# Performance work log

Measured on AMD Instinct MI355X. Metric: run time of the kernel, lower is better.

## Reference

```python
import jax, jax.numpy as jnp
import numpy as np

B, H, S, D = 2, 8, 2048, 64

def setup_inputs() -> dict:
    key = jax.random.key(0)
    ks = jax.random.split(key, 6)
    names = ["Qx", "Kx", "Vx", "Qy", "Ky", "Vy"]
    return {n: jax.random.normal(k, (B, H, S, D), dtype=jnp.float32)
            for n, k in zip(names, ks)}

def reference(Qx, Kx, Vx, Qy, Ky, Vy):
    scale = float(np.sqrt(Qx.shape[-1]))
    # Two score matmuls: [B,H,S,S] each
    ax = jnp.einsum('bhqd,bhkd->bhqk', Qx, Kx)
    ay = jnp.einsum('bhqd,bhkd->bhqk', Qy, Ky)
    # cat(dim=1) -> reshape(B,2,H,S,S) -> mean(dim=1) == elementwise average
    attn = (ax + ay) * 0.5
    # numerically stable softmax over keys; dropout is identity in eval mode
    w = jax.nn.softmax(attn / scale, axis=-1)
    # Shared attention weights into two value matmuls
    out1 = jnp.einsum('bhqk,bhkd->bhqd', w, Vx)
    out2 = jnp.einsum('bhqk,bhkd->bhqd', w, Vy)
    return (out1, out2)
```

## Files before the change

kernel.cpp:

```cpp
#include <hip/hip_runtime.h>
#include <hip/hip_bf16.h>

typedef __attribute__((ext_vector_type(4)))  float f32x4;
typedef __attribute__((ext_vector_type(16))) float f32x16;
typedef __attribute__((ext_vector_type(8)))  short s16x8;
typedef __attribute__((ext_vector_type(4)))  short s16x4;
typedef __attribute__((ext_vector_type(4)))  int   i32x4;

#define BB 2
#define HH 8
#define SS 2048
#define DD 64
#define QBLK 128
#define NT   32
#define NT2  16
#define NBH  (BB * HH)

#define WS_KX 0
#define WS_KY ((size_t)NBH * NT * 8192)
#define WS_VX ((size_t)2 * NBH * NT * 8192)
#define WS_VY ((size_t)3 * NBH * NT * 8192)
#define WS_NEED ((size_t)4 * NBH * NT * 8192)

__device__ __forceinline__ short f2bf(float x) {
    unsigned u = __builtin_bit_cast(unsigned, x);
    u = (u + 0x7FFFu + ((u >> 16) & 1u)) >> 16;
    return (short)u;
}

__device__ __forceinline__ unsigned cvtpk(float lo, float hi) {
    unsigned d;
    asm("v_cvt_pk_bf16_f32 %0, %1, %2" : "=v"(d) : "v"(lo), "v"(hi));
    return d;
}

__device__ __forceinline__ int swz(int row, int byteInRow) {
    return row * 128 + (byteInRow ^ ((row & 7) << 4));
}

__device__ __forceinline__ void glds16(const void* g, void* l) {
    __builtin_amdgcn_global_load_lds(
        (const __attribute__((address_space(1))) unsigned*)g,
        (__attribute__((address_space(3))) unsigned*)l, 16, 0, 0);
}

__global__ __launch_bounds__(256)
void prep_kv(const float* __restrict__ Kx, const float* __restrict__ Ky,
             const float* __restrict__ Vx, const float* __restrict__ Vy,
             char* __restrict__ ws)
{
    const int b = blockIdx.x;
    if (b < 1024) {
        const int tid  = b * 256 + threadIdx.x;
        const int dblk = tid & 7;
        const int s    = (tid >> 3) & 2047;
        const int bh   = tid >> 14;
        const size_t gi = ((size_t)bh * SS + s) * DD + dblk * 8;
        const int kt = s >> 6, row = s & 63;
        const size_t dst = (size_t)(bh * NT + kt) * 8192 + swz(row, dblk * 16);
        const float* px = Kx + gi;
        const float* py = Ky + gi;
        s16x8 a, bb;
#pragma unroll
        for (int i = 0; i < 8; ++i) { a[i] = f2bf(px[i]); bb[i] = f2bf(py[i]); }
        *(s16x8*)(ws + WS_KX + dst) = a;
        *(s16x8*)(ws + WS_KY + dst) = bb;
    } else {
        const int tid  = (b - 1024) * 256 + threadIdx.x;
        const int d    = tid & 63;
        const int sblk = (tid >> 6) & 7;
        const int kt   = (tid >> 9) & 31;
        const int bh   = tid >> 14;
        const size_t gbase = ((size_t)bh * SS + kt * 64 + sblk * 8) * DD + d;
        s16x8 a, bb;
#pragma unroll
        for (int i = 0; i < 8; ++i) {
            a[i]  = f2bf(Vx[gbase + (size_t)i * DD]);
            bb[i] = f2bf(Vy[gbase + (size_t)i * DD]);
        }
        const size_t dst = (size_t)(bh * NT + kt) * 8192 + swz(d, sblk * 16);
        *(s16x8*)(ws + WS_VX + dst) = a;
        *(s16x8*)(ws + WS_VY + dst) = bb;
    }
}

__global__ __launch_bounds__(512, 2)
void attn_main(const float* __restrict__ Qx, const float* __restrict__ Qy,
               const char* __restrict__ ws, float* __restrict__ Out)
{
    extern __shared__ char lds[];

    const int t    = threadIdx.x;
    const int lane = t & 63;
    const int w    = t >> 6;
    const int qsub = w & 3;
    const int ks   = w >> 2;
    const int l31  = lane & 31;
    const int hi   = lane >> 5;

    int bid = blockIdx.x;
    bid = (bid & 7) * 32 + (bid >> 3);
    const int bh = bid >> 4;
    const int q0 = (bid & 15) * QBLK;
    const size_t base = (size_t)bh * SS * DD;

    const int qrow = q0 + qsub * 32 + l31;
    s16x8 qbx[4], qby[4];
#pragma unroll
    for (int dc = 0; dc < 4; ++dc) {
        const int d0 = dc * 16 + hi * 8;
        const float* qp = Qx + base + (size_t)qrow * DD + d0;
        const float* qq = Qy + base + (size_t)qrow * DD + d0;
        const float4 f0 = *(const float4*)qp;
        const float4 f1 = *(const float4*)(qp + 4);
        const float4 h0 = *(const float4*)qq;
        const float4 h1 = *(const float4*)(qq + 4);
        qbx[dc][0]=f2bf(f0.x); qbx[dc][1]=f2bf(f0.y); qbx[dc][2]=f2bf(f0.z); qbx[dc][3]=f2bf(f0.w);
        qbx[dc][4]=f2bf(f1.x); qbx[dc][5]=f2bf(f1.y); qbx[dc][6]=f2bf(f1.z); qbx[dc][7]=f2bf(f1.w);
        qby[dc][0]=f2bf(h0.x); qby[dc][1]=f2bf(h0.y); qby[dc][2]=f2bf(h0.z); qby[dc][3]=f2bf(h0.w);
        qby[dc][4]=f2bf(h1.x); qby[dc][5]=f2bf(h1.y); qby[dc][6]=f2bf(h1.z); qby[dc][7]=f2bf(h1.w);
    }

    f32x16 o1_0, o1_1, o2_0, o2_1;
#pragma unroll
    for (int j = 0; j < 16; ++j) { o1_0[j] = 0.f; o1_1[j] = 0.f; o2_0[j] = 0.f; o2_1[j] = 0.f; }
    float lsum = 0.f;

    const float SCL = 0.09016844005556021f;

#define STAGE(kt_, b_)                                                             \
    do {                                                                           \
        const size_t img_ = (size_t)(bh * NT + (kt_) * 2) * 8192 + (size_t)t * 16; \
        char* dst_ = lds + (b_) * 65536 + t * 16;                                  \
        glds16(ws + WS_KX + img_,        dst_);                                    \
        glds16(ws + WS_KX + img_ + 8192, dst_ + 8192);                             \
        glds16(ws + WS_KY + img_,        dst_ + 16384);                            \
        glds16(ws + WS_KY + img_ + 8192, dst_ + 24576);                            \
        glds16(ws + WS_VX + img_,        dst_ + 32768);                            \
        glds16(ws + WS_VX + img_ + 8192, dst_ + 40960);                            \
        glds16(ws + WS_VY + img_,        dst_ + 49152);                            \
        glds16(ws + WS_VY + img_ + 8192, dst_ + 57344);                            \
    } while (0)

#define QK_BLOCK(buf_, h_, sc_)                                                    \
    do {                                                                           \
        const char* KxI_ = (buf_) + ks * 8192;                                     \
        const char* KyI_ = (buf_) + 16384 + ks * 8192;                             \
        _Pragma("unroll")                                                          \
        for (int dc = 0; dc < 4; ++dc) {                                           \
            const int off = swz((h_) * 32 + l31, dc * 32 + hi * 16);               \
            const s16x8 ka = *(const s16x8*)(KxI_ + off);                          \
            const s16x8 kb = *(const s16x8*)(KyI_ + off);                          \
            sc_ = __builtin_amdgcn_mfma_f32_32x32x16_bf16(ka, qbx[dc], sc_, 0, 0, 0); \
            sc_ = __builtin_amdgcn_mfma_f32_32x32x16_bf16(kb, qby[dc], sc_, 0, 0, 0); \
        }                                                                          \
    } while (0)

#define V_READS(buf_, h_, vr_)                                                     \
    do {                                                                           \
        const char* VxI_ = (buf_) + 32768 + ks * 8192;                             \
        const char* VyI_ = (buf_) + 49152 + ks * 8192;                             \
        _Pragma("unroll")                                                          \
        for (int ch = 0; ch < 2; ++ch) {                                           \
            const int off0 = swz(l31,      (h_) * 64 + ch * 32 + hi * 16);         \
            const int off1 = swz(32 + l31, (h_) * 64 + ch * 32 + hi * 16);         \
            vr_[ch * 4 + 0] = *(const s16x8*)(VxI_ + off0);                        \
            vr_[ch * 4 + 1] = *(const s16x8*)(VxI_ + off1);                        \
            vr_[ch * 4 + 2] = *(const s16x8*)(VyI_ + off0);                        \
            vr_[ch * 4 + 3] = *(const s16x8*)(VyI_ + off1);                        \
        }                                                                          \
    } while (0)

#define SOFTMAX_PA(sc_, pa_)                                                       \
    do {                                                                           \
        float s_ = 0.f;                                                            \
        _Pragma("unroll")                                                          \
        for (int j = 0; j < 16; ++j) { sc_[j] = exp2f(sc_[j] * SCL); s_ += sc_[j]; } \
        lsum += s_;                                                                \
        _Pragma("unroll")                                                          \
        for (int ch = 0; ch < 2; ++ch) {                                           \
            const int b8 = ch * 8;                                                 \
            unsigned x0 = cvtpk(sc_[b8 + 0], sc_[b8 + 1]);                         \
            unsigned x1 = cvtpk(sc_[b8 + 2], sc_[b8 + 3]);                         \
            unsigned y0 = cvtpk(sc_[b8 + 4], sc_[b8 + 5]);                         \
            unsigned y1 = cvtpk(sc_[b8 + 6], sc_[b8 + 7]);                         \
            asm("v_permlane32_swap_b32 %0, %1" : "+v"(x0), "+v"(y0));              \
            asm("v_permlane32_swap_b32 %0, %1" : "+v"(x1), "+v"(y1));              \
            i32x4 pw;                                                              \
            pw[0] = (int)x0; pw[1] = (int)x1; pw[2] = (int)y0; pw[3] = (int)y1;    \
            pa_[ch] = __builtin_bit_cast(s16x8, pw);                               \
        }                                                                          \
    } while (0)

#define PV_BLOCK(pa_, vr_)                                                         \
    do {                                                                           \
        _Pragma("unroll")                                                          \
        for (int ch = 0; ch < 2; ++ch) {                                           \
            o1_0 = __builtin_amdgcn_mfma_f32_32x32x16_bf16(pa_[ch], vr_[ch*4+0], o1_0, 0, 0, 0); \
            o1_1 = __builtin_amdgcn_mfma_f32_32x32x16_bf16(pa_[ch], vr_[ch*4+1], o1_1, 0, 0, 0); \
            o2_0 = __builtin_amdgcn_mfma_f32_32x32x16_bf16(pa_[ch], vr_[ch*4+2], o2_0, 0, 0, 0); \
            o2_1 = __builtin_amdgcn_mfma_f32_32x32x16_bf16(pa_[ch], vr_[ch*4+3], o2_1, 0, 0, 0); \
        }                                                                          \
    } while (0)

#define ZERO16(v_) { _Pragma("unroll") for (int j = 0; j < 16; ++j) (v_)[j] = 0.f; }

    STAGE(0, 0);
    __syncthreads();
    int cur = 0;

    for (int kt = 0; kt < NT2; ++kt) {
        if (kt + 1 < NT2) STAGE(kt + 1, cur ^ 1);

        const char* buf = lds + cur * 65536;
        f32x16 scA, scB;
        ZERO16(scA); ZERO16(scB);
        s16x8 pa[2], vrA[8], vrB[8];

        __builtin_amdgcn_s_setprio(1);
        QK_BLOCK(buf, 0, scA);
        QK_BLOCK(buf, 1, scB);
        V_READS(buf, 0, vrA);
        SOFTMAX_PA(scA, pa);
        PV_BLOCK(pa, vrA);
        V_READS(buf, 1, vrB);
        SOFTMAX_PA(scB, pa);
        PV_BLOCK(pa, vrB);
        __builtin_amdgcn_s_setprio(0);

        __syncthreads();
        cur ^= 1;
    }

#undef STAGE
#undef QK_BLOCK
#undef V_READS
#undef SOFTMAX_PA
#undef PV_BLOCK
#undef ZERO16

    const float lh = lsum + __shfl_xor(lsum, 32);

    __syncthreads();
    float* ex   = (float*)lds;
    float* linv = (float*)(lds + 65536);
    const int exo = (qsub * 64 + lane) * 33;
    float* O1 = Out;
    float* O2 = Out + (size_t)BB * HH * SS * DD;

    if (ks == 1) {
#pragma unroll
        for (int j = 0; j < 16; ++j) { ex[exo + j] = o1_0[j]; ex[exo + 16 + j] = o1_1[j]; }
        ex[exo + 32] = lh;
    }
    __syncthreads();
    if (ks == 0 && hi == 0)
        linv[qsub * 32 + l31] = 1.0f / (lh + ex[exo + 32]);
    __syncthreads();
    if (ks == 0) {
#pragma unroll
        for (int j = 0; j < 16; ++j) {
            const int qr = (j & 3) + 8 * (j >> 2) + 4 * hi;
            const float invj = linv[qsub * 32 + qr];
            const size_t ob = base + (size_t)(q0 + qsub * 32 + qr) * DD + l31;
            O1[ob]      = (o1_0[j] + ex[exo + j])      * invj;
            O1[ob + 32] = (o1_1[j] + ex[exo + 16 + j]) * invj;
        }
    }
    __syncthreads();
    if (ks == 1) {
#pragma unroll
        for (int j = 0; j < 16; ++j) { ex[exo + j] = o2_0[j]; ex[exo + 16 + j] = o2_1[j]; }
    }
    __syncthreads();
    if (ks == 0) {
#pragma unroll
        for (int j = 0; j < 16; ++j) {
            const int qr = (j & 3) + 8 * (j >> 2) + 4 * hi;
            const float invj = linv[qsub * 32 + qr];
            const size_t ob = base + (size_t)(q0 + qsub * 32 + qr) * DD + l31;
            O2[ob]      = (o2_0[j] + ex[exo + j])      * invj;
            O2[ob + 32] = (o2_1[j] + ex[exo + 16 + j]) * invj;
        }
    }
}

__global__ __launch_bounds__(256, 2)
void attn_dual_fallback(const float* __restrict__ Qx, const float* __restrict__ Kx,
                        const float* __restrict__ Vx, const float* __restrict__ Qy,
                        const float* __restrict__ Ky, const float* __restrict__ Vy,
                        float* __restrict__ Out)
{
    __shared__ __attribute__((aligned(16))) char lds[40960];
    char* KxL  = lds;
    char* KyL  = lds + 8192;
    char* VtxL = lds + 16384;
    char* VtyL = lds + 24576;

    const int t    = threadIdx.x;
    const int lane = t & 63;
    const int w    = t >> 6;
    const int g    = lane >> 4;
    const int c    = lane & 15;
    char* PL = lds + 32768 + w * 2048;

    const int bid = blockIdx.x;
    const int bh  = bid >> 5;
    const int q0  = (bid & 31) * 64;
    const size_t base = (size_t)bh * SS * DD;

    const int qrowA = q0 + w * 16 + c;
    s16x8 qxf[2], qyf[2];
#pragma unroll
    for (int kk = 0; kk < 2; ++kk) {
        const int d0 = kk * 32 + g * 8;
        const float* qp = Qx + base + (size_t)qrowA * DD + d0;
        const float* qq = Qy + base + (size_t)qrowA * DD + d0;
#pragma unroll
        for (int i = 0; i < 8; ++i) { qxf[kk][i] = f2bf(qp[i]); qyf[kk][i] = f2bf(qq[i]); }
    }

    f32x4 o1[4], o2[4];
#pragma unroll
    for (int n = 0; n < 4; ++n) {
        o1[n] = (f32x4){0.f, 0.f, 0.f, 0.f};
        o2[n] = (f32x4){0.f, 0.f, 0.f, 0.f};
    }
    float m[4]    = {-1e30f, -1e30f, -1e30f, -1e30f};
    float lsum[4] = {0.f, 0.f, 0.f, 0.f};
    const float SCL = 0.09016844005556021f;

    for (int kt = 0; kt < SS / 64; ++kt) {
        __syncthreads();
#pragma unroll
        for (int j = 0; j < 4; ++j) {
            const int f   = t + 256 * j;
            const int row = f >> 4;
            const int c4  = f & 15;
            const size_t gi = base + (size_t)(kt * 64 + row) * DD + c4 * 4;
            const float4 kx = *(const float4*)(Kx + gi);
            const float4 ky = *(const float4*)(Ky + gi);
            const float4 vx = *(const float4*)(Vx + gi);
            const float4 vy = *(const float4*)(Vy + gi);
            s16x4 a; a[0]=f2bf(kx.x); a[1]=f2bf(kx.y); a[2]=f2bf(kx.z); a[3]=f2bf(kx.w);
            *(s16x4*)(KxL + swz(row, c4 * 8)) = a;
            s16x4 b; b[0]=f2bf(ky.x); b[1]=f2bf(ky.y); b[2]=f2bf(ky.z); b[3]=f2bf(ky.w);
            *(s16x4*)(KyL + swz(row, c4 * 8)) = b;
            const int d0 = c4 * 4;
            *(short*)(VtxL + swz(d0 + 0, row * 2)) = f2bf(vx.x);
            *(short*)(VtxL + swz(d0 + 1, row * 2)) = f2bf(vx.y);
            *(short*)(VtxL + swz(d0 + 2, row * 2)) = f2bf(vx.z);
            *(short*)(VtxL + swz(d0 + 3, row * 2)) = f2bf(vx.w);
            *(short*)(VtyL + swz(d0 + 0, row * 2)) = f2bf(vy.x);
            *(short*)(VtyL + swz(d0 + 1, row * 2)) = f2bf(vy.y);
            *(short*)(VtyL + swz(d0 + 2, row * 2)) = f2bf(vy.z);
            *(short*)(VtyL + swz(d0 + 3, row * 2)) = f2bf(vy.w);
        }
        __syncthreads();

        f32x4 sc[4];
#pragma unroll
        for (int n = 0; n < 4; ++n) {
            f32x4 acc = (f32x4){0.f, 0.f, 0.f, 0.f};
            const int keyrow = n * 16 + c;
#pragma unroll
            for (int kk = 0; kk < 2; ++kk) {
                const int off = swz(keyrow, (kk * 32 + g * 8) * 2);
                const s16x8 kxf = *(const s16x8*)(KxL + off);
                const s16x8 kyf = *(const s16x8*)(KyL + off);
                acc = __builtin_amdgcn_mfma_f32_16x16x32_bf16(qxf[kk], kxf, acc, 0, 0, 0);
                acc = __builtin_amdgcn_mfma_f32_16x16x32_bf16(qyf[kk], kyf, acc, 0, 0, 0);
            }
            sc[n] = acc;
        }

#pragma unroll
        for (int r = 0; r < 4; ++r) {
            float v0 = fmaxf(fmaxf(sc[0][r], sc[1][r]), fmaxf(sc[2][r], sc[3][r])) * SCL;
#pragma unroll
            for (int off = 1; off < 16; off <<= 1) v0 = fmaxf(v0, __shfl_xor(v0, off));
            const float mnew = fmaxf(m[r], v0);
            const float cr = exp2f(m[r] - mnew);
            m[r] = mnew;
            float srow = 0.f;
#pragma unroll
            for (int n = 0; n < 4; ++n) {
                const float pp = exp2f(sc[n][r] * SCL - mnew);
                srow += pp;
                *(short*)(PL + swz(g * 4 + r, (n * 16 + c) * 2)) = f2bf(pp);
            }
#pragma unroll
            for (int off = 1; off < 16; off <<= 1) srow += __shfl_xor(srow, off);
            lsum[r] = lsum[r] * cr + srow;
#pragma unroll
            for (int n = 0; n < 4; ++n) { o1[n][r] *= cr; o2[n][r] *= cr; }
        }

        s16x8 pf[2];
#pragma unroll
        for (int kk = 0; kk < 2; ++kk)
            pf[kk] = *(const s16x8*)(PL + swz(c, (kk * 32 + g * 8) * 2));
#pragma unroll
        for (int nd = 0; nd < 4; ++nd) {
            const int drow = nd * 16 + c;
#pragma unroll
            for (int kk = 0; kk < 2; ++kk) {
                const int off = swz(drow, (kk * 32 + g * 8) * 2);
                const s16x8 vxf = *(const s16x8*)(VtxL + off);
                const s16x8 vyf = *(const s16x8*)(VtyL + off);
                o1[nd] = __builtin_amdgcn_mfma_f32_16x16x32_bf16(pf[kk], vxf, o1[nd], 0, 0, 0);
                o2[nd] = __builtin_amdgcn_mfma_f32_16x16x32_bf16(pf[kk], vyf, o2[nd], 0, 0, 0);
            }
        }
    }

    float* O1 = Out;
    float* O2 = Out + (size_t)BB * HH * SS * DD;
#pragma unroll
    for (int r = 0; r < 4; ++r) {
        const float inv = 1.0f / lsum[r];
        const int qrow = q0 + w * 16 + g * 4 + r;
        const size_t ob = base + (size_t)qrow * DD + c;
#pragma unroll
        for (int nd = 0; nd < 4; ++nd) {
            O1[ob + nd * 16] = o1[nd][r] * inv;
            O2[ob + nd * 16] = o2[nd][r] * inv;
        }
    }
}

extern "C" void kernel_launch(void* const* d_in, const int* in_sizes, int n_in,
                              void* d_out, int out_size, void* d_ws, size_t ws_size,
                              hipStream_t stream) {
    const float* Qx = (const float*)d_in[0];
    const float* Kx = (const float*)d_in[1];
    const float* Vx = (const float*)d_in[2];
    const float* Qy = (const float*)d_in[3];
    const float* Ky = (const float*)d_in[4];
    const float* Vy = (const float*)d_in[5];
    float* Out = (float*)d_out;

    if (ws_size >= WS_NEED) {
        char* ws = (char*)d_ws;
        hipLaunchKernelGGL(prep_kv, dim3(2048), dim3(256), 0, stream,
                           Kx, Ky, Vx, Vy, ws);
        hipFuncSetAttribute((const void*)attn_main,
                            hipFuncAttributeMaxDynamicSharedMemorySize, 131072);
        hipLaunchKernelGGL(attn_main, dim3(NBH * (SS / QBLK)), dim3(512), 131072,
                           stream, Qx, Qy, (const char*)ws, Out);
    } else {
        hipLaunchKernelGGL(attn_dual_fallback, dim3(NBH * 32), dim3(256),
                           0, stream, Qx, Kx, Vx, Qy, Ky, Vy, Out);
    }
}
```

Measured before the change: 59.46 us.

## Split key tiles four ways across 16 waves per attention block

Each block grows from 512 to 1024 threads. The 64-key tile is now split across four wave groups of 32 keys each instead of two groups processing two 32-key halves in sequence. Staging issues half as many async global-to-LDS loads per thread, and the epilogue reduces three partial output/sum sets through LDS instead of one. The aim is more waves per CU to hide latency and shorter per-wave dependency chains, at the cost of tighter register budgets (possible spills), a larger reduction epilogue and more barrier participants.

```diff
diff --git a/kernel.cpp b/kernel.cpp
--- a/kernel.cpp
+++ b/kernel.cpp
@@ -84,7 +84,7 @@
     }
 }
 
-__global__ __launch_bounds__(512, 2)
+__global__ __launch_bounds__(1024, 4)
 void attn_main(const float* __restrict__ Qx, const float* __restrict__ Qy,
                const char* __restrict__ ws, float* __restrict__ Out)
 {
@@ -128,27 +128,27 @@
 
     const float SCL = 0.09016844005556021f;
 
+    const int kimg = (ks >> 1) * 8192;
+    const int krow = (ks & 1) * 32 + l31;
+    const int kbyt = (ks & 1) * 64;
+
 #define STAGE(kt_, b_)                                                             \
     do {                                                                           \
         const size_t img_ = (size_t)(bh * NT + (kt_) * 2) * 8192 + (size_t)t * 16; \
         char* dst_ = lds + (b_) * 65536 + t * 16;                                  \
-        glds16(ws + WS_KX + img_,        dst_);                                    \
-        glds16(ws + WS_KX + img_ + 8192, dst_ + 8192);                             \
-        glds16(ws + WS_KY + img_,        dst_ + 16384);                            \
-        glds16(ws + WS_KY + img_ + 8192, dst_ + 24576);                            \
-        glds16(ws + WS_VX + img_,        dst_ + 32768);                            \
-        glds16(ws + WS_VX + img_ + 8192, dst_ + 40960);                            \
-        glds16(ws + WS_VY + img_,        dst_ + 49152);                            \
-        glds16(ws + WS_VY + img_ + 8192, dst_ + 57344);                            \
+        glds16(ws + WS_KX + img_, dst_);                                           \
+        glds16(ws + WS_KY + img_, dst_ + 16384);                                   \
+        glds16(ws + WS_VX + img_, dst_ + 32768);                                   \
+        glds16(ws + WS_VY + img_, dst_ + 49152);                                   \
     } while (0)
 
-#define QK_BLOCK(buf_, h_, sc_)                                                    \
+#define QK_BLOCK(buf_, sc_)                                                        \
     do {                                                                           \
-        const char* KxI_ = (buf_) + ks * 8192;                                     \
-        const char* KyI_ = (buf_) + 16384 + ks * 8192;                             \
+        const char* KxI_ = (buf_) + kimg;                                          \
+        const char* KyI_ = (buf_) + 16384 + kimg;                                  \
         _Pragma("unroll")                                                          \
         for (int dc = 0; dc < 4; ++dc) {                                           \
-            const int off = swz((h_) * 32 + l31, dc * 32 + hi * 16);               \
+            const int off = swz(krow, dc * 32 + hi * 16);                          \
             const s16x8 ka = *(const s16x8*)(KxI_ + off);                          \
             const s16x8 kb = *(const s16x8*)(KyI_ + off);                          \
             sc_ = __builtin_amdgcn_mfma_f32_32x32x16_bf16(ka, qbx[dc], sc_, 0, 0, 0); \
@@ -156,14 +156,14 @@
         }                                                                          \
     } while (0)
 
-#define V_READS(buf_, h_, vr_)                                                     \
+#define V_READS(buf_, vr_)                                                         \
     do {                                                                           \
-        const char* VxI_ = (buf_) + 32768 + ks * 8192;                             \
-        const char* VyI_ = (buf_) + 49152 + ks * 8192;                             \
+        const char* VxI_ = (buf_) + 32768 + kimg;                                  \
+        const char* VyI_ = (buf_) + 49152 + kimg;                                  \
         _Pragma("unroll")                                                          \
         for (int ch = 0; ch < 2; ++ch) {                                           \
-            const int off0 = swz(l31,      (h_) * 64 + ch * 32 + hi * 16);         \
-            const int off1 = swz(32 + l31, (h_) * 64 + ch * 32 + hi * 16);         \
+            const int off0 = swz(l31,      kbyt + ch * 32 + hi * 16);              \
+            const int off1 = swz(32 + l31, kbyt + ch * 32 + hi * 16);              \
             vr_[ch * 4 + 0] = *(const s16x8*)(VxI_ + off0);                        \
             vr_[ch * 4 + 1] = *(const s16x8*)(VxI_ + off1);                        \
             vr_[ch * 4 + 2] = *(const s16x8*)(VyI_ + off0);                        \
@@ -213,19 +213,15 @@
         if (kt + 1 < NT2) STAGE(kt + 1, cur ^ 1);
 
         const char* buf = lds + cur * 65536;
-        f32x16 scA, scB;
-        ZERO16(scA); ZERO16(scB);
-        s16x8 pa[2], vrA[8], vrB[8];
+        f32x16 sc;
+        ZERO16(sc);
+        s16x8 pa[2], vr[8];
 
         __builtin_amdgcn_s_setprio(1);
-        QK_BLOCK(buf, 0, scA);
-        QK_BLOCK(buf, 1, scB);
-        V_READS(buf, 0, vrA);
-        SOFTMAX_PA(scA, pa);
-        PV_BLOCK(pa, vrA);
-        V_READS(buf, 1, vrB);
-        SOFTMAX_PA(scB, pa);
-        PV_BLOCK(pa, vrB);
+        QK_BLOCK(buf, sc);
+        V_READS(buf, vr);
+        SOFTMAX_PA(sc, pa);
+        PV_BLOCK(pa, vr);
         __builtin_amdgcn_s_setprio(0);
 
         __syncthreads();
@@ -243,32 +239,44 @@
 
     __syncthreads();
     float* ex   = (float*)lds;
-    float* linv = (float*)(lds + 65536);
-    const int exo = (qsub * 64 + lane) * 33;
+    float* linv = (float*)(lds + 110592);
+    const int exo = (((ks - 1) * 4 + qsub) * 64 + lane) * 33;
     float* O1 = Out;
     float* O2 = Out + (size_t)BB * HH * SS * DD;
 
-    if (ks == 1) {
+    if (ks != 0) {
 #pragma unroll
         for (int j = 0; j < 16; ++j) { ex[exo + j] = o1_0[j]; ex[exo + 16 + j] = o1_1[j]; }
         ex[exo + 32] = lh;
     }
     __syncthreads();
-    if (ks == 0 && hi == 0)
-        linv[qsub * 32 + l31] = 1.0f / (lh + ex[exo + 32]);
+    if (ks == 0 && hi == 0) {
+        float ltot = lh;
+#pragma unroll
+        for (int kk = 1; kk < 4; ++kk)
+            ltot += ex[(((kk - 1) * 4 + qsub) * 64 + lane) * 33 + 32];
+        linv[qsub * 32 + l31] = 1.0f / ltot;
+    }
     __syncthreads();
     if (ks == 0) {
 #pragma unroll
         for (int j = 0; j < 16; ++j) {
             const int qr = (j & 3) + 8 * (j >> 2) + 4 * hi;
             const float invj = linv[qsub * 32 + qr];
+            float a0 = o1_0[j], a1 = o1_1[j];
+#pragma unroll
+            for (int kk = 1; kk < 4; ++kk) {
+                const int eo = (((kk - 1) * 4 + qsub) * 64 + lane) * 33;
+                a0 += ex[eo + j];
+                a1 += ex[eo + 16 + j];
+            }
             const size_t ob = base + (size_t)(q0 + qsub * 32 + qr) * DD + l31;
-            O1[ob]      = (o1_0[j] + ex[exo + j])      * invj;
-            O1[ob + 32] = (o1_1[j] + ex[exo + 16 + j]) * invj;
-        }
-    }
-    __syncthreads();
-    if (ks == 1) {
+            O1[ob]      = a0 * invj;
+            O1[ob + 32] = a1 * invj;
+        }
+    }
+    __syncthreads();
+    if (ks != 0) {
 #pragma unroll
         for (int j = 0; j < 16; ++j) { ex[exo + j] = o2_0[j]; ex[exo + 16 + j] = o2_1[j]; }
     }
@@ -278,9 +286,16 @@
         for (int j = 0; j < 16; ++j) {
             const int qr = (j & 3) + 8 * (j >> 2) + 4 * hi;
             const float invj = linv[qsub * 32 + qr];
+            float a0 = o2_0[j], a1 = o2_1[j];
+#pragma unroll
+            for (int kk = 1; kk < 4; ++kk) {
+                const int eo = (((kk - 1) * 4 + qsub) * 64 + lane) * 33;
+                a0 += ex[eo + j];
+                a1 += ex[eo + 16 + j];
+            }
             const size_t ob = base + (size_t)(q0 + qsub * 32 + qr) * DD + l31;
-            O2[ob]      = (o2_0[j] + ex[exo + j])      * invj;
-            O2[ob + 32] = (o2_1[j] + ex[exo + 16 + j]) * invj;
+            O2[ob]      = a0 * invj;
+            O2[ob + 32] = a1 * invj;
         }
     }
 }
@@ -446,7 +461,7 @@
                            Kx, Ky, Vx, Vy, ws);
         hipFuncSetAttribute((const void*)attn_main,
                             hipFuncAttributeMaxDynamicSharedMemorySize, 131072);
-        hipLaunchKernelGGL(attn_main, dim3(NBH * (SS / QBLK)), dim3(512), 131072,
+        hipLaunchKernelGGL(attn_main, dim3(NBH * (SS / QBLK)), dim3(1024), 131072,
                            stream, Qx, Qy, (const char*)ws, Out);
     } else {
         hipLaunchKernelGGL(attn_dual_fallback, dim3(NBH * 32), dim3(256),
```

New measurement: 73.53 us. 23.7% more time.

## Switch to 4-slot smaller K/V tiles with 3-deep prefetch and folded Q scaling

Applied to the files above, without the earlier changes.

Replaces the 2-buffer 64KB staging of two key tiles per iteration with a 4-slot ring of 32KB single-tile buffers, keeping three tiles in flight. Explicit vmcnt waits plus a single barrier per iteration replace the trailing __syncthreads. The softmax scale is folded into Q before the bf16 conversion, which removes a multiply per score element. This adds more barriers per key, since there are twice as many iterations, and slightly changes rounding because the scale is applied before bf16 conversion.

```diff
diff --git a/kernel.cpp b/kernel.cpp
--- a/kernel.cpp
+++ b/kernel.cpp
@@ -13,7 +13,6 @@
 #define DD 64
 #define QBLK 128
 #define NT   32
-#define NT2  16
 #define NBH  (BB * HH)
 
 #define WS_KX 0
@@ -104,6 +103,8 @@
     const int q0 = (bid & 15) * QBLK;
     const size_t base = (size_t)bh * SS * DD;
 
+    const float SCL = 0.09016844005556021f;
+
     const int qrow = q0 + qsub * 32 + l31;
     s16x8 qbx[4], qby[4];
 #pragma unroll
@@ -115,10 +116,10 @@
         const float4 f1 = *(const float4*)(qp + 4);
         const float4 h0 = *(const float4*)qq;
         const float4 h1 = *(const float4*)(qq + 4);
-        qbx[dc][0]=f2bf(f0.x); qbx[dc][1]=f2bf(f0.y); qbx[dc][2]=f2bf(f0.z); qbx[dc][3]=f2bf(f0.w);
-        qbx[dc][4]=f2bf(f1.x); qbx[dc][5]=f2bf(f1.y); qbx[dc][6]=f2bf(f1.z); qbx[dc][7]=f2bf(f1.w);
-        qby[dc][0]=f2bf(h0.x); qby[dc][1]=f2bf(h0.y); qby[dc][2]=f2bf(h0.z); qby[dc][3]=f2bf(h0.w);
-        qby[dc][4]=f2bf(h1.x); qby[dc][5]=f2bf(h1.y); qby[dc][6]=f2bf(h1.z); qby[dc][7]=f2bf(h1.w);
+        qbx[dc][0]=f2bf(f0.x*SCL); qbx[dc][1]=f2bf(f0.y*SCL); qbx[dc][2]=f2bf(f0.z*SCL); qbx[dc][3]=f2bf(f0.w*SCL);
+        qbx[dc][4]=f2bf(f1.x*SCL); qbx[dc][5]=f2bf(f1.y*SCL); qbx[dc][6]=f2bf(f1.z*SCL); qbx[dc][7]=f2bf(f1.w*SCL);
+        qby[dc][0]=f2bf(h0.x*SCL); qby[dc][1]=f2bf(h0.y*SCL); qby[dc][2]=f2bf(h0.z*SCL); qby[dc][3]=f2bf(h0.w*SCL);
+        qby[dc][4]=f2bf(h1.x*SCL); qby[dc][5]=f2bf(h1.y*SCL); qby[dc][6]=f2bf(h1.z*SCL); qby[dc][7]=f2bf(h1.w*SCL);
     }
 
     f32x16 o1_0, o1_1, o2_0, o2_1;
@@ -126,29 +127,23 @@
     for (int j = 0; j < 16; ++j) { o1_0[j] = 0.f; o1_1[j] = 0.f; o2_0[j] = 0.f; o2_1[j] = 0.f; }
     float lsum = 0.f;
 
-    const float SCL = 0.09016844005556021f;
-
 #define STAGE(kt_, b_)                                                             \
     do {                                                                           \
-        const size_t img_ = (size_t)(bh * NT + (kt_) * 2) * 8192 + (size_t)t * 16; \
-        char* dst_ = lds + (b_) * 65536 + t * 16;                                  \
-        glds16(ws + WS_KX + img_,        dst_);                                    \
-        glds16(ws + WS_KX + img_ + 8192, dst_ + 8192);                             \
-        glds16(ws + WS_KY + img_,        dst_ + 16384);                            \
-        glds16(ws + WS_KY + img_ + 8192, dst_ + 24576);                            \
-        glds16(ws + WS_VX + img_,        dst_ + 32768);                            \
-        glds16(ws + WS_VX + img_ + 8192, dst_ + 40960);                            \
-        glds16(ws + WS_VY + img_,        dst_ + 49152);                            \
-        glds16(ws + WS_VY + img_ + 8192, dst_ + 57344);                            \
+        const size_t img_ = (size_t)(bh * NT + (kt_)) * 8192 + (size_t)t * 16;     \
+        char* dst_ = lds + (b_) * 32768 + (t & 511) * 16;                          \
+        glds16(ws + WS_KX + img_, dst_);                                           \
+        glds16(ws + WS_KY + img_, dst_ + 8192);                                    \
+        glds16(ws + WS_VX + img_, dst_ + 16384);                                   \
+        glds16(ws + WS_VY + img_, dst_ + 24576);                                   \
     } while (0)
 
-#define QK_BLOCK(buf_, h_, sc_)                                                    \
+#define QK_BLOCK(buf_, sc_)                                                        \
     do {                                                                           \
-        const char* KxI_ = (buf_) + ks * 8192;                                     \
-        const char* KyI_ = (buf_) + 16384 + ks * 8192;                             \
+        const char* KxI_ = (buf_);                                                 \
+        const char* KyI_ = (buf_) + 8192;                                          \
         _Pragma("unroll")                                                          \
         for (int dc = 0; dc < 4; ++dc) {                                           \
-            const int off = swz((h_) * 32 + l31, dc * 32 + hi * 16);               \
+            const int off = swz(ks * 32 + l31, dc * 32 + hi * 16);                 \
             const s16x8 ka = *(const s16x8*)(KxI_ + off);                          \
             const s16x8 kb = *(const s16x8*)(KyI_ + off);                          \
             sc_ = __builtin_amdgcn_mfma_f32_32x32x16_bf16(ka, qbx[dc], sc_, 0, 0, 0); \
@@ -156,14 +151,14 @@
         }                                                                          \
     } while (0)
 
-#define V_READS(buf_, h_, vr_)                                                     \
+#define V_READS(buf_, vr_)                                                         \
     do {                                                                           \
-        const char* VxI_ = (buf_) + 32768 + ks * 8192;                             \
-        const char* VyI_ = (buf_) + 49152 + ks * 8192;                             \
+        const char* VxI_ = (buf_) + 16384;                                         \
+        const char* VyI_ = (buf_) + 24576;                                         \
         _Pragma("unroll")                                                          \
         for (int ch = 0; ch < 2; ++ch) {                                           \
-            const int off0 = swz(l31,      (h_) * 64 + ch * 32 + hi * 16);         \
-            const int off1 = swz(32 + l31, (h_) * 64 + ch * 32 + hi * 16);         \
+            const int off0 = swz(l31,      ks * 64 + ch * 32 + hi * 16);           \
+            const int off1 = swz(32 + l31, ks * 64 + ch * 32 + hi * 16);           \
             vr_[ch * 4 + 0] = *(const s16x8*)(VxI_ + off0);                        \
             vr_[ch * 4 + 1] = *(const s16x8*)(VxI_ + off1);                        \
             vr_[ch * 4 + 2] = *(const s16x8*)(VyI_ + off0);                        \
@@ -175,7 +170,7 @@
     do {                                                                           \
         float s_ = 0.f;                                                            \
         _Pragma("unroll")                                                          \
-        for (int j = 0; j < 16; ++j) { sc_[j] = exp2f(sc_[j] * SCL); s_ += sc_[j]; } \
+        for (int j = 0; j < 16; ++j) { sc_[j] = exp2f(sc_[j]); s_ += sc_[j]; }     \
         lsum += s_;                                                                \
         _Pragma("unroll")                                                          \
         for (int ch = 0; ch < 2; ++ch) {                                           \
@@ -206,30 +201,27 @@
 #define ZERO16(v_) { _Pragma("unroll") for (int j = 0; j < 16; ++j) (v_)[j] = 0.f; }
 
     STAGE(0, 0);
-    __syncthreads();
-    int cur = 0;
-
-    for (int kt = 0; kt < NT2; ++kt) {
-        if (kt + 1 < NT2) STAGE(kt + 1, cur ^ 1);
-
-        const char* buf = lds + cur * 65536;
-        f32x16 scA, scB;
-        ZERO16(scA); ZERO16(scB);
-        s16x8 pa[2], vrA[8], vrB[8];
+    STAGE(1, 1);
+    STAGE(2, 2);
+
+    for (int kt = 0; kt < NT; ++kt) {
+        if (kt < NT - 2)      asm volatile("s_waitcnt vmcnt(8)" ::: "memory");
+        else if (kt == NT - 2) asm volatile("s_waitcnt vmcnt(4)" ::: "memory");
+        else                   asm volatile("s_waitcnt vmcnt(0)" ::: "memory");
+        __builtin_amdgcn_s_barrier();
+        if (kt + 3 < NT) STAGE(kt + 3, (kt + 3) & 3);
+
+        const char* buf = lds + (kt & 3) * 32768;
+        f32x16 sc;
+        ZERO16(sc);
+        s16x8 pa[2], vr[8];
 
         __builtin_amdgcn_s_setprio(1);
-        QK_BLOCK(buf, 0, scA);
-        QK_BLOCK(buf, 1, scB);
-        V_READS(buf, 0, vrA);
-        SOFTMAX_PA(scA, pa);
-        PV_BLOCK(pa, vrA);
-        V_READS(buf, 1, vrB);
-        SOFTMAX_PA(scB, pa);
-        PV_BLOCK(pa, vrB);
+        V_READS(buf, vr);
+        QK_BLOCK(buf, sc);
+        SOFTMAX_PA(sc, pa);
+        PV_BLOCK(pa, vr);
         __builtin_amdgcn_s_setprio(0);
-
-        __syncthreads();
-        cur ^= 1;
     }
 
 #undef STAGE
```

Result: slower. 60.84 us (+2.3%).
